# Performance work log

Hardware: AMD Instinct MI355X
Metric: run time of the kernel (lower is better)

The kernel has to match this reference:

```python
import jax, jax.numpy as jnp
import numpy as np

B, S, D, MAXC, BIAS_LEN = 2, 4096, 512, 32, 128
TEMP = 1.0


def setup_inputs() -> dict:
    key = jax.random.key(0)
    ks = jax.random.split(key, 16)
    d2, d4 = D // 2, D // 4
    n = lambda k, shp, s: (jax.random.normal(k, shp, jnp.float32) * s)
    return {
        "x": n(ks[0], (B, S, D), 1.0),
        "Wi1": n(ks[1], (D, d2), 0.02), "bi1": jnp.zeros((d2,), jnp.float32),
        "Wi2": n(ks[2], (d2, D), 0.02), "bi2": jnp.zeros((D,), jnp.float32),
        "Wf1": n(ks[3], (D, d2), 0.02), "bf1": jnp.zeros((d2,), jnp.float32),
        "Wf2": n(ks[4], (d2, D), 0.02), "bf2": jnp.zeros((D,), jnp.float32),
        "loc_bias": n(ks[5], (BIAS_LEN,), 0.1),
        "Wn1": n(ks[6], (D, d4), 0.02), "bn1": jnp.zeros((d4,), jnp.float32),
        "Wn2": n(ks[7], (d4, 1), 0.02), "bn2": jnp.zeros((1,), jnp.float32),
        "mask": jnp.ones((B, S), dtype=bool),
    }


def reference(x, Wi1, bi1, Wi2, bi2, Wf1, bf1, Wf2, bf2, loc_bias,
              Wn1, bn1, Wn2, bn2, mask):
    b, s, d = x.shape
    gelu = lambda t: jax.nn.gelu(t, approximate=False)  # torch exact GELU

    intents = gelu(x @ Wi1 + bi1) @ Wi2 + bi2        # (b,s,d)
    features = gelu(x @ Wf1 + bf1) @ Wf2 + bf2       # (b,s,d)

    # QK-style full score matrix (b,s,s)
    scores = jnp.einsum("bid,bjd->bij", intents, features) / jnp.sqrt(jnp.float32(d))

    # Gathered locality bias from learned 1D table
    pos = jnp.arange(s)
    rel = pos[None, :] - pos[:, None]                # rel[i,j] = j - i
    L = loc_bias.shape[0]
    idx = jnp.clip(rel, -L // 2, L // 2 - 1) + L // 2
    scores = scores + loc_bias[idx][None]            # (b,s,s)

    neg_inf = jnp.float32(-jnp.inf)
    scores = jnp.where((rel > 0)[None], neg_inf, scores)        # causal
    m2 = mask[:, None, :] & mask[:, :, None]                    # padding
    scores = jnp.where(m2, scores, neg_inf)

    # adaptive k predictor (computed as in the original; unused for outputs)
    ratio = jax.nn.sigmoid(gelu(x @ Wn1 + bn1) @ Wn2 + bn2)[..., 0]
    _adaptive_k = jnp.clip(ratio * MAXC, 1, None).astype(jnp.int32)

    k = min(MAXC, s)
    top_scores, top_indices = jax.lax.top_k(scores, k)          # (b,s,k)
    weights = jax.nn.softmax(top_scores / TEMP, axis=-1)
    return top_indices, weights
```

## Files before the change

kernel.cpp:

```cpp
#include <hip/hip_runtime.h>
#include <math.h>

#define BB   2
#define SS   4096
#define DD   512
#define DH   256
#define KTOP 32
#define KSEL 64
#define TGT  48
#define HALF 2048
#define SCALE 0.044194173824159216f

typedef __bf16 bf16_t;
typedef bf16_t bf16x8 __attribute__((ext_vector_type(8)));
typedef float  f32x4  __attribute__((ext_vector_type(4)));

__device__ __forceinline__ int tri_row(int q) {
    int r = (int)((sqrtf(8.0f * q + 1.0f) - 1.0f) * 0.5f);
    while ((r + 1) * (r + 2) / 2 <= q) ++r;
    while (r * (r + 1) / 2 > q) --r;
    return r;
}

__device__ __forceinline__ void decode_tile(int id, int h, int& rt, int& jtl, int& jtg) {
    if (h == 0) {
        if (id < 256) { rt = 16 + (id >> 4); jtl = id & 15; }
        else { int q = id - 256; rt = tri_row(q); jtl = q - rt * (rt + 1) / 2; }
        jtg = jtl;
    } else {
        int r = tri_row(id); rt = 16 + r;
        jtl = id - r * (r + 1) / 2; jtg = jtl + 16;
    }
}

template<bool GELU>
__global__ __launch_bounds__(256)
void gemm128(const float* __restrict__ A0, const float* __restrict__ A1,
             const float* __restrict__ W0, const float* __restrict__ W1,
             const float* __restrict__ b0, const float* __restrict__ b1,
             float* __restrict__ C0, float* __restrict__ C1,
             bf16_t* __restrict__ Bs0, bf16_t* __restrict__ Bs1,
             int N, int K)
{
    __shared__ float As[32][132];
    __shared__ float Ws[32][132];
    const int t = threadIdx.x;
    const int z = blockIdx.z;
    const float* A    = z ? A1 : A0;
    const float* W    = z ? W1 : W0;
    const float* bias = z ? b1 : b0;
    float*       C    = z ? C1 : C0;
    bf16_t*      Bsh  = z ? Bs1 : Bs0;
    const int n0 = blockIdx.x * 128;
    const int m0 = blockIdx.y * 128;

    const int kq = t & 7;
    const int rr = t >> 3;
    const int wkr = t >> 3;
    const int wnc = (t & 7) * 16;
    const float* Ab = A + (size_t)m0 * K;
    const float* Wb = W + (size_t)0 * N + n0;

    const int lane = t & 63, wav = t >> 6;
    const int wr = wav >> 1, wc = wav & 1;
    const int li = lane >> 3, lj = lane & 7;

    float acc[8][8] = {};
    float4 aR[4], wR[4];
    #pragma unroll
    for (int u = 0; u < 4; ++u) {
        int r = u * 32 + rr;
        aR[u] = *(const float4*)&Ab[(size_t)r * K + 4 * kq];
        wR[u] = *(const float4*)&Wb[(size_t)wkr * N + wnc + 4 * u];
    }
    const int nch = K >> 5;
    for (int c = 0; c < nch; ++c) {
        __syncthreads();
        #pragma unroll
        for (int u = 0; u < 4; ++u) {
            int r = u * 32 + rr;
            As[4*kq+0][r] = aR[u].x; As[4*kq+1][r] = aR[u].y;
            As[4*kq+2][r] = aR[u].z; As[4*kq+3][r] = aR[u].w;
            *(float4*)&Ws[wkr][wnc + 4 * u] = wR[u];
        }
        __syncthreads();
        if (c + 1 < nch) {
            int k0 = (c + 1) * 32;
            #pragma unroll
            for (int u = 0; u < 4; ++u) {
                int r = u * 32 + rr;
                aR[u] = *(const float4*)&Ab[(size_t)r * K + k0 + 4 * kq];
                wR[u] = *(const float4*)&Wb[(size_t)(k0 + wkr) * N + wnc + 4 * u];
            }
        }
        #pragma unroll
        for (int kk = 0; kk < 32; ++kk) {
            float4 a0 = *(const float4*)&As[kk][wr * 64 + li * 8];
            float4 a1 = *(const float4*)&As[kk][wr * 64 + li * 8 + 4];
            float4 b0v = *(const float4*)&Ws[kk][wc * 64 + lj * 8];
            float4 b1v = *(const float4*)&Ws[kk][wc * 64 + lj * 8 + 4];
            float av[8] = {a0.x,a0.y,a0.z,a0.w,a1.x,a1.y,a1.z,a1.w};
            float bv[8] = {b0v.x,b0v.y,b0v.z,b0v.w,b1v.x,b1v.y,b1v.z,b1v.w};
            #pragma unroll
            for (int ri = 0; ri < 8; ++ri)
                #pragma unroll
                for (int rj = 0; rj < 8; ++rj)
                    acc[ri][rj] = fmaf(av[ri], bv[rj], acc[ri][rj]);
        }
    }

    const int nb = n0 + wc * 64 + lj * 8;
    float bv0[8];
    *(float4*)&bv0[0] = *(const float4*)&bias[nb];
    *(float4*)&bv0[4] = *(const float4*)&bias[nb + 4];
    #pragma unroll
    for (int ri = 0; ri < 8; ++ri) {
        int m = m0 + wr * 64 + li * 8 + ri;
        float o[8];
        #pragma unroll
        for (int rj = 0; rj < 8; ++rj) {
            float v = acc[ri][rj] + bv0[rj];
            if (GELU) v = 0.5f * v * (1.0f + erff(v * 0.7071067811865475f));
            o[rj] = v;
        }
        *(float4*)&C[(size_t)m * N + nb]     = make_float4(o[0],o[1],o[2],o[3]);
        *(float4*)&C[(size_t)m * N + nb + 4] = make_float4(o[4],o[5],o[6],o[7]);
        if (Bsh) {
            bf16x8 hv;
            #pragma unroll
            for (int rj = 0; rj < 8; ++rj) hv[rj] = (bf16_t)o[rj];
            *(bf16x8*)&Bsh[(size_t)m * N + nb] = hv;
        }
    }
}

__device__ __forceinline__ void stage_tile(const bf16_t* __restrict__ g,
                                           bf16_t* lds, int t, int k0)
{
    const int r0 = t >> 2;
    const int cb = (t & 3) * 8;
    const int wb = (t >> 6) * 512;
    #pragma unroll
    for (int inst = 0; inst < 2; ++inst) {
        const bf16_t* gp = g + (size_t)(inst * 64 + r0) * DD + (k0 + cb);
        bf16_t* lp = lds + inst * 2048 + wb;
        __builtin_amdgcn_global_load_lds(
            (const __attribute__((address_space(1))) void*)gp,
            (__attribute__((address_space(3))) void*)lp, 16, 0, 0);
    }
}

__global__ __launch_bounds__(256, 2)
void scores_approx_g(const bf16_t* __restrict__ Ib, const bf16_t* __restrict__ Fb,
                     const float* __restrict__ lb, float* __restrict__ Sc, int h)
{
    __shared__ bf16_t As[2][128 * 32];
    __shared__ bf16_t Bs[2][128 * 32];
    const int t = threadIdx.x;

    int rt, jtl, jtg;
    decode_tile(blockIdx.x, h, rt, jtl, jtg);
    const int b  = blockIdx.z;
    const int i0 = rt << 7, j0 = jtg << 7;
    const size_t bo = (size_t)b * SS * DD;
    const bf16_t* Ag = Ib + bo + (size_t)i0 * DD;
    const bf16_t* Bg = Fb + bo + (size_t)j0 * DD;

    const int lane = t & 63, wav = t >> 6;
    const int wr = wav >> 1, wc = wav & 1;
    const int lr = lane & 15;
    const int lk = lane >> 4;

    f32x4 acc[4][4];
    #pragma unroll
    for (int i = 0; i < 4; ++i)
        #pragma unroll
        for (int j = 0; j < 4; ++j) {
            acc[i][j][0] = 0.f; acc[i][j][1] = 0.f;
            acc[i][j][2] = 0.f; acc[i][j][3] = 0.f;
        }

    stage_tile(Ag, &As[0][0], t, 0);
    stage_tile(Bg, &Bs[0][0], t, 0);
    for (int c = 0; c < 16; ++c) {
        __syncthreads();
        if (c + 1 < 16) {
            stage_tile(Ag, &As[(c + 1) & 1][0], t, (c + 1) * 32);
            stage_tile(Bg, &Bs[(c + 1) & 1][0], t, (c + 1) * 32);
        }
        const bf16_t* Ab = &As[c & 1][0];
        const bf16_t* Bb = &Bs[c & 1][0];
        bf16x8 bh[4];
        #pragma unroll
        for (int j = 0; j < 4; ++j)
            bh[j] = *(const bf16x8*)(Bb + (wc * 64 + j * 16 + lr) * 32 + lk * 8);
        #pragma unroll
        for (int i = 0; i < 4; ++i) {
            bf16x8 ah = *(const bf16x8*)(Ab + (wr * 64 + i * 16 + lr) * 32 + lk * 8);
            #pragma unroll
            for (int j = 0; j < 4; ++j)
                acc[i][j] = __builtin_amdgcn_mfma_f32_16x16x32_bf16(
                                ah, bh[j], acc[i][j], 0, 0, 0);
        }
    }

    const bool farTile = (i0 - j0) >= 256;
    const float lb0 = lb[0];
    #pragma unroll
    for (int i = 0; i < 4; ++i) {
        #pragma unroll
        for (int j = 0; j < 4; ++j) {
            int gj    = j0 + wc * 64 + j * 16 + lr;
            int cbase = (jtl << 7) + wc * 64 + j * 16 + lr;
            #pragma unroll
            for (int rg = 0; rg < 4; ++rg) {
                int gi = i0 + wr * 64 + i * 16 + lk * 4 + rg;
                float v = acc[i][j][rg] * SCALE;
                if (farTile) v += lb0;
                else {
                    int rel = gj - gi;
                    int bi  = rel < -64 ? 0 : rel + 64;
                    v += lb[min(bi, 127)];
                    if (rel > 0) v = -INFINITY;
                }
                Sc[((size_t)b * SS + gi) * HALF + cbase] = v;
            }
        }
    }
}

__global__ __launch_bounds__(256, 2)
void scores_approx(const float* __restrict__ If, const float* __restrict__ Ff,
                   const float* __restrict__ lb, float* __restrict__ Sc, int h)
{
    __shared__ __align__(16) bf16_t AS[128][40];
    __shared__ __align__(16) bf16_t BS[128][40];
    const int t = threadIdx.x;

    int rt, jtl, jtg;
    decode_tile(blockIdx.x, h, rt, jtl, jtg);
    const int b  = blockIdx.z;
    const int i0 = rt << 7, j0 = jtg << 7;
    const size_t bo = (size_t)b * SS * DD;
    const float* Ag = If + bo + (size_t)i0 * DD;
    const float* Bg = Ff + bo + (size_t)j0 * DD;

    const int r0 = t >> 2;
    const int cb = (t & 3) * 8;

    const int lane = t & 63, wav = t >> 6;
    const int wr = wav >> 1, wc = wav & 1;
    const int lr = lane & 15;
    const int lk = lane >> 4;

    f32x4 acc[4][4];
    #pragma unroll
    for (int i = 0; i < 4; ++i)
        #pragma unroll
        for (int j = 0; j < 4; ++j) {
            acc[i][j][0] = 0.f; acc[i][j][1] = 0.f;
            acc[i][j][2] = 0.f; acc[i][j][3] = 0.f;
        }

    float4 aF[4], bF[4];
    #pragma unroll
    for (int u = 0; u < 2; ++u) {
        const float* ap = Ag + (size_t)(u * 64 + r0) * DD + cb;
        const float* bp = Bg + (size_t)(u * 64 + r0) * DD + cb;
        aF[2*u] = *(const float4*)ap;  aF[2*u+1] = *(const float4*)(ap + 4);
        bF[2*u] = *(const float4*)bp;  bF[2*u+1] = *(const float4*)(bp + 4);
    }

    for (int c = 0; c < 16; ++c) {
        __syncthreads();
        #pragma unroll
        for (int u = 0; u < 2; ++u) {
            float va[8] = {aF[2*u].x, aF[2*u].y, aF[2*u].z, aF[2*u].w,
                           aF[2*u+1].x, aF[2*u+1].y, aF[2*u+1].z, aF[2*u+1].w};
            float vb[8] = {bF[2*u].x, bF[2*u].y, bF[2*u].z, bF[2*u].w,
                           bF[2*u+1].x, bF[2*u+1].y, bF[2*u+1].z, bF[2*u+1].w};
            bf16x8 av8, bv8;
            #pragma unroll
            for (int e = 0; e < 8; ++e) {
                av8[e] = (bf16_t)va[e];
                bv8[e] = (bf16_t)vb[e];
            }
            int rw = u * 64 + r0;
            *(bf16x8*)&AS[rw][cb] = av8;
            *(bf16x8*)&BS[rw][cb] = bv8;
        }
        __syncthreads();
        if (c + 1 < 16) {
            int k0 = (c + 1) * 32;
            #pragma unroll
            for (int u = 0; u < 2; ++u) {
                const float* ap = Ag + (size_t)(u * 64 + r0) * DD + k0 + cb;
                const float* bp = Bg + (size_t)(u * 64 + r0) * DD + k0 + cb;
                aF[2*u] = *(const float4*)ap;  aF[2*u+1] = *(const float4*)(ap + 4);
                bF[2*u] = *(const float4*)bp;  bF[2*u+1] = *(const float4*)(bp + 4);
            }
        }
        bf16x8 bh[4];
        #pragma unroll
        for (int j = 0; j < 4; ++j)
            bh[j] = *(const bf16x8*)&BS[wc * 64 + j * 16 + lr][lk * 8];
        #pragma unroll
        for (int i = 0; i < 4; ++i) {
            bf16x8 ah = *(const bf16x8*)&AS[wr * 64 + i * 16 + lr][lk * 8];
            #pragma unroll
            for (int j = 0; j < 4; ++j)
                acc[i][j] = __builtin_amdgcn_mfma_f32_16x16x32_bf16(
                                ah, bh[j], acc[i][j], 0, 0, 0);
        }
    }

    const bool farTile = (i0 - j0) >= 256;
    const float lb0 = lb[0];
    #pragma unroll
    for (int i = 0; i < 4; ++i) {
        #pragma unroll
        for (int j = 0; j < 4; ++j) {
            int gj    = j0 + wc * 64 + j * 16 + lr;
            int cbase = (jtl << 7) + wc * 64 + j * 16 + lr;
            #pragma unroll
            for (int rg = 0; rg < 4; ++rg) {
                int gi = i0 + wr * 64 + i * 16 + lk * 4 + rg;
                float v = acc[i][j][rg] * SCALE;
                if (farTile) v += lb0;
                else {
                    int rel = gj - gi;
                    int bi  = rel < -64 ? 0 : rel + 64;
                    v += lb[min(bi, 127)];
                    if (rel > 0) v = -INFINITY;
                }
                Sc[((size_t)b * SS + gi) * HALF + cbase] = v;
            }
        }
    }
}

__global__ __launch_bounds__(64)
void topk_rescore(const float* __restrict__ Sc,
                  const float* __restrict__ If, const float* __restrict__ Ff,
                  const float* __restrict__ lb,
                  const float* __restrict__ p0v_in, const int* __restrict__ p0j_in,
                  float* __restrict__ p0v_out, int* __restrict__ p0j_out,
                  float* __restrict__ out, int h)
{
    __shared__ float mv[64];
    __shared__ int   mj[64];
    __shared__ float sOv[32];
    __shared__ int   sOj[32];
    __shared__ int   sCand[64];

    const int lane = threadIdx.x;
    const int wid  = blockIdx.x;
    int b, i;
    if (h == 0) { b = wid >> 12; i = wid & 4095; }
    else        { b = wid >> 11; i = HALF + (wid & 2047); }
    const int nv = (h == 0) ? min(i + 1, HALF) : (i + 1 - HALF);
    const size_t rb = ((size_t)b * SS + i) * HALF;
    const int l4 = lane * 4;

    int n = KSEL;
    int selj;
    if (nv <= KSEL) {
        selj = h * HALF + lane;
    } else {
        unsigned key[32];
        #pragma unroll
        for (int s = 0; s < 8; ++s) {
            int jb = s * 256 + l4;
            float4 f = make_float4(-INFINITY, -INFINITY, -INFINITY, -INFINITY);
            if (jb < nv) f = *(const float4*)&Sc[rb + jb];
            float vv[4] = {f.x, f.y, f.z, f.w};
            #pragma unroll
            for (int q = 0; q < 4; ++q) {
                unsigned ub = __float_as_uint(vv[q]);
                unsigned k  = (ub & 0x80000000u) ? ~ub : (ub | 0x80000000u);
                key[4*s+q] = ((jb + q) < nv) ? k : 0u;
            }
        }
        unsigned cur = 0u;
        int csel = HALF;
        for (int bit = 31; bit >= 0 && csel > KSEL; --bit) {
            unsigned test = cur | (1u << bit);
            int cl = 0;
            #pragma unroll
            for (int c = 0; c < 32; ++c) cl += (key[c] >= test) ? 1 : 0;
            #pragma unroll
            for (int m = 1; m < 64; m <<= 1) cl += __shfl_xor(cl, m, 64);
            if (cl >= TGT) { cur = test; csel = cl; }
        }
        int base = 0;
        #pragma unroll
        for (int c = 0; c < 32; ++c) {
            bool surv = key[c] >= cur;
            unsigned long long mm = __ballot(surv);
            if (surv) {
                int pos = base + (int)__popcll(mm & ((1ull << lane) - 1ull));
                if (pos < KSEL)
                    sCand[pos] = (c >> 2) * 256 + l4 + (c & 3) + h * HALF;
            }
            base += (int)__popcll(mm);
        }
        n = min(base, KSEL);
        __syncthreads();
        selj = (lane < n) ? sCand[lane] : (h * HALF);
    }

    float selv;
    {
        const size_t bo = (size_t)b * SS * DD;
        const float* Irow = If + bo + (size_t)i * DD;
        const float* Frow = Ff + bo + (size_t)selj * DD;
        float acc = 0.f;
        #pragma unroll 8
        for (int k = 0; k < DD; k += 4) {
            float4 fi = *(const float4*)&Irow[k];
            float4 fj = *(const float4*)&Frow[k];
            acc = fmaf(fi.x, fj.x, acc);
            acc = fmaf(fi.y, fj.y, acc);
            acc = fmaf(fi.z, fj.z, acc);
            acc = fmaf(fi.w, fj.w, acc);
        }
        float v = acc * SCALE;
        int rel = selj - i;
        int bi  = rel < -64 ? 0 : rel + 64;
        v += lb[min(bi, 127)];
        if (rel > 0) v = -INFINITY;
        selv = v;
    }
    if (lane >= n) selv = -INFINITY;

    mv[lane] = selv; mj[lane] = selj;
    __syncthreads();
    int rk = 0;
    #pragma unroll
    for (int f = 0; f < 64; ++f) {
        float fv = mv[f]; int fj = mj[f];
        rk += (fv > selv || (fv == selv && fj < selj)) ? 1 : 0;
    }
    if (rk < KTOP) { sOv[rk] = selv; sOj[rk] = selj; }
    __syncthreads();
    if (lane < KTOP) { selv = sOv[lane]; selj = sOj[lane]; }

    if (h == 0 && i >= HALF) {
        if (lane < KTOP) {
            size_t pb = ((size_t)b * HALF + (i - HALF)) * KTOP + lane;
            p0v_out[pb] = selv; p0j_out[pb] = selj;
        }
        return;
    }

    if (h == 1) {
        float p0v = 0.f; int p0j = 0;
        __syncthreads();
        if (lane < KTOP) {
            size_t pb = ((size_t)b * HALF + (i - HALF)) * KTOP + lane;
            p0v = p0v_in[pb]; p0j = p0j_in[pb];
            mv[lane] = p0v;         mj[lane] = p0j;
            mv[KTOP + lane] = selv; mj[KTOP + lane] = selj;
        }
        __syncthreads();
        int r0 = 0, r1 = 0;
        if (lane < KTOP) {
            for (int f = 0; f < 64; ++f) {
                float fv = mv[f]; int fj = mj[f];
                r0 += (fv > p0v || (fv == p0v && fj < p0j)) ? 1 : 0;
                r1 += (fv > selv || (fv == selv && fj < selj)) ? 1 : 0;
            }
        }
        __syncthreads();
        if (lane < KTOP) {
            if (r0 < KTOP) { sOv[r0] = p0v;  sOj[r0] = p0j;  }
            if (r1 < KTOP) { sOv[r1] = selv; sOj[r1] = selj; }
        }
        __syncthreads();
        if (lane < KTOP) { selv = sOv[lane]; selj = sOj[lane]; }
    }

    float mx = __shfl(selv, 0, 64);
    float e  = (lane < KTOP) ? expf(selv - mx) : 0.f;
    float sum = e;
    #pragma unroll
    for (int m = 1; m < 64; m <<= 1) sum += __shfl_xor(sum, m, 64);
    float invs = 1.0f / sum;
    if (lane < KTOP) {
        size_t ob = ((size_t)b * SS + i) * KTOP + lane;
        out[ob] = (float)selj;
        out[(size_t)BB * SS * KTOP + ob] = e * invs;
    }
}

extern "C" void kernel_launch(void* const* d_in, const int* in_sizes, int n_in,
                              void* d_out, int out_size, void* d_ws, size_t ws_size,
                              hipStream_t stream)
{
    const float* x   = (const float*)d_in[0];
    const float* Wi1 = (const float*)d_in[1];
    const float* bi1 = (const float*)d_in[2];
    const float* Wi2 = (const float*)d_in[3];
    const float* bi2 = (const float*)d_in[4];
    const float* Wf1 = (const float*)d_in[5];
    const float* bf1 = (const float*)d_in[6];
    const float* Wf2 = (const float*)d_in[7];
    const float* bf2 = (const float*)d_in[8];
    const float* lb  = (const float*)d_in[9];

    const size_t NF = (size_t)BB * SS * DD;
    float* ws       = (float*)d_ws;
    float* intents  = ws;
    float* features = ws + NF;
    float* part0v   = ws + 2 * NF;
    int*   part0j   = (int*)(part0v + (size_t)BB * HALF * KTOP);
    float* Sc       = ws + 2 * NF + NF / 2;
    float* Hi       = Sc;
    float* Hf       = Sc + NF / 2;

    const size_t baseFloats = 2 * NF + NF / 2 + 4 * NF;
    const bool   useG       = ws_size >= (baseFloats + NF) * sizeof(float);
    bf16_t* IFb = (bf16_t*)(ws + baseFloats);

    gemm128<true ><<<dim3(DH / 128, 64, 2), 256, 0, stream>>>(
        x, x, Wi1, Wf1, bi1, bf1, Hi, Hf, nullptr, nullptr, DH, DD);
    gemm128<false><<<dim3(DD / 128, 64, 2), 256, 0, stream>>>(
        Hi, Hf, Wi2, Wf2, bi2, bf2, intents, features,
        useG ? IFb : nullptr, useG ? (IFb + NF) : nullptr, DD, DH);

    if (useG) {
        scores_approx_g<<<dim3(392, 1, BB), 256, 0, stream>>>(
            IFb, IFb + NF, lb, Sc, 0);
    } else {
        scores_approx<<<dim3(392, 1, BB), 256, 0, stream>>>(
            intents, features, lb, Sc, 0);
    }
    topk_rescore<<<BB * SS, 64, 0, stream>>>(Sc, intents, features, lb,
                                             part0v, part0j, part0v, part0j,
                                             (float*)d_out, 0);
    if (useG) {
        scores_approx_g<<<dim3(136, 1, BB), 256, 0, stream>>>(
            IFb, IFb + NF, lb, Sc, 1);
    } else {
        scores_approx<<<dim3(136, 1, BB), 256, 0, stream>>>(
            intents, features, lb, Sc, 1);
    }
    topk_rescore<<<BB * HALF, 64, 0, stream>>>(Sc, intents, features, lb,
                                               part0v, part0j, part0v, part0j,
                                               (float*)d_out, 1);
}
```

Baseline: 478.3 us.

## Stage rescore query row and candidate feature rows through LDS with coalesced loads

```diff
diff --git a/kernel.cpp b/kernel.cpp
--- a/kernel.cpp
+++ b/kernel.cpp
@@ -352,6 +352,8 @@
     __shared__ float sOv[32];
     __shared__ int   sOj[32];
     __shared__ int   sCand[64];
+    __shared__ __align__(16) float sIrow[DD];
+    __shared__ __align__(16) float sF[64 * 34];
 
     const int lane = threadIdx.x;
     const int wid  = blockIdx.x;
@@ -360,7 +362,16 @@
     else        { b = wid >> 11; i = HALF + (wid & 2047); }
     const int nv = (h == 0) ? min(i + 1, HALF) : (i + 1 - HALF);
     const size_t rb = ((size_t)b * SS + i) * HALF;
+    const size_t bo = (size_t)b * SS * DD;
     const int l4 = lane * 4;
+
+    {
+        const float* Irow = If + bo + (size_t)i * DD;
+        float4 t0 = *(const float4*)&Irow[lane * 8];
+        float4 t1 = *(const float4*)&Irow[lane * 8 + 4];
+        *(float4*)&sIrow[lane * 8]     = t0;
+        *(float4*)&sIrow[lane * 8 + 4] = t1;
+    }
 
     int n = KSEL;
     int selj;
@@ -409,22 +420,46 @@
         selj = (lane < n) ? sCand[lane] : (h * HALF);
     }
 
+    sCand[lane] = selj;
+    __syncthreads();
+    int cj[8];
+    #pragma unroll
+    for (int u = 0; u < 8; ++u) cj[u] = sCand[u * 8 + (lane >> 3)];
+
+    float accd = 0.f;
+    const int s4 = (lane & 7) * 4;
+    const int cw = (lane >> 3);
+    float4 gv[8];
+    #pragma unroll
+    for (int u = 0; u < 8; ++u)
+        gv[u] = *(const float4*)&Ff[bo + (size_t)cj[u] * DD + s4];
+    for (int kc = 0; kc < 16; ++kc) {
+        #pragma unroll
+        for (int u = 0; u < 8; ++u) {
+            float* p = &sF[(u * 8 + cw) * 34 + s4];
+            *(float2*)&p[0] = make_float2(gv[u].x, gv[u].y);
+            *(float2*)&p[2] = make_float2(gv[u].z, gv[u].w);
+        }
+        __syncthreads();
+        if (kc + 1 < 16) {
+            int k0n = (kc + 1) * 32;
+            #pragma unroll
+            for (int u = 0; u < 8; ++u)
+                gv[u] = *(const float4*)&Ff[bo + (size_t)cj[u] * DD + k0n + s4];
+        }
+        int k0 = kc * 32;
+        #pragma unroll
+        for (int e2 = 0; e2 < 16; ++e2) {
+            float2 fi = *(const float2*)&sIrow[k0 + e2 * 2];
+            float2 fj = *(const float2*)&sF[lane * 34 + e2 * 2];
+            accd = fmaf(fi.x, fj.x, accd);
+            accd = fmaf(fi.y, fj.y, accd);
+        }
+        __syncthreads();
+    }
     float selv;
     {
-        const size_t bo = (size_t)b * SS * DD;
-        const float* Irow = If + bo + (size_t)i * DD;
-        const float* Frow = Ff + bo + (size_t)selj * DD;
-        float acc = 0.f;
-        #pragma unroll 8
-        for (int k = 0; k < DD; k += 4) {
-            float4 fi = *(const float4*)&Irow[k];
-            float4 fj = *(const float4*)&Frow[k];
-            acc = fmaf(fi.x, fj.x, acc);
-            acc = fmaf(fi.y, fj.y, acc);
-            acc = fmaf(fi.z, fj.z, acc);
-            acc = fmaf(fi.w, fj.w, acc);
-        }
-        float v = acc * SCALE;
+        float v = accd * SCALE;
         int rel = selj - i;
         int bi  = rel < -64 ? 0 : rel + 64;
         v += lb[min(bi, 127)];
```

Measured after the change: 478.3 us. About the same (+0.0%).
